# Performance work log

Hardware: AMD Instinct MI355X
Metric: run time of the kernel (lower is better)

## Reference

```python
import jax, jax.numpy as jnp
import numpy as np

NC, K, SD = 8, 1024, 64
L = NC * SD
B = 8192
TAU = 0.07
COMMIT_W = 1.0
CONTRAST_W = 1.0
EPS = 1e-12


def setup_inputs() -> dict:
    key = jax.random.key(0)
    kz, ke = jax.random.split(key)
    z = jax.random.normal(kz, (B, L), dtype=jnp.float32)
    embeddings = jax.random.normal(ke, (NC, K, SD), dtype=jnp.float32)
    return {"z": z, "embeddings": embeddings}


def reference(z, embeddings):
    sg = jax.lax.stop_gradient
    Bn, Ln = z.shape
    nc, k, sd = embeddings.shape
    zr = z.reshape(Bn, nc, sd)  # (B, nc, sd)

    # squared distances via ||z||^2 - 2 z.e + ||e||^2 -> (B, nc, K), avoids (B,nc,K,sd)
    z2 = jnp.sum(zr * zr, axis=-1)[:, :, None]
    e2 = jnp.sum(embeddings * embeddings, axis=-1)[None, :, :]
    cross = jnp.einsum('bnd,nkd->bnk', zr, embeddings)
    dists = z2 - 2.0 * cross + e2
    indices = jnp.argmin(dists, axis=-1)  # (B, nc)

    # codebook gather
    quant_splits = embeddings[jnp.arange(nc)[None, :], indices]  # (B, nc, sd)
    quant_z = quant_splits.reshape(Bn, Ln)

    commit_loss = jnp.mean((sg(quant_z) - z) ** 2)
    embed_loss = jnp.mean((quant_z - sg(z)) ** 2)
    total_commit = commit_loss + embed_loss

    quant_z_st = z + sg(quant_z - z)

    z_norm = z / jnp.maximum(jnp.linalg.norm(z, axis=-1, keepdims=True), EPS)
    q_det = sg(quant_z)
    q_norm = q_det / jnp.maximum(jnp.linalg.norm(q_det, axis=-1, keepdims=True), EPS)
    logits = jnp.matmul(q_norm, z_norm.T) / TAU  # (B, B)
    # cross-entropy with labels = arange(B)
    contrastive = jnp.mean(jax.nn.logsumexp(logits, axis=1) - jnp.diagonal(logits))

    return (quant_z_st, COMMIT_W * total_commit, CONTRAST_W * contrastive, indices)
```

## Files before the change

kernel.cpp:

```cpp
#include <hip/hip_runtime.h>
#include <cstdint>
#include <cstddef>

#define NCB   8
#define KC    1024
#define SDIM  64
#define LDIM  512
#define BATCH 8192
#define INV_TAU (1.0f/0.07f)
#define K2E  20.60992915555662f
#define DBIAS 256.0f

typedef __bf16 bf16_t;
typedef bf16_t bf16x8 __attribute__((ext_vector_type(8)));
typedef float  floatx4 __attribute__((ext_vector_type(4)));
typedef int    intx8  __attribute__((ext_vector_type(8)));
typedef unsigned int u32;

__device__ __forceinline__ unsigned short f2bf(float f) {
    union { float f; unsigned int u; } c; c.f = f;
    unsigned int u = c.u;
    u += 0x7fffu + ((u >> 16) & 1u);
    return (unsigned short)(u >> 16);
}
__device__ __forceinline__ float bf2f(unsigned short h) {
    union { unsigned int u; float f; } c; c.u = ((unsigned int)h) << 16;
    return c.f;
}
__device__ __forceinline__ float exp2_fast(float x) {
    float r; asm("v_exp_f32 %0, %1" : "=v"(r) : "v"(x)); return r;
}
__device__ __forceinline__ void gll16(const void* g, void* l) {
    __builtin_amdgcn_global_load_lds(
        (const __attribute__((address_space(1))) u32*)g,
        (__attribute__((address_space(3))) u32*)l,
        16, 0, 0);
}

__global__ __launch_bounds__(256) void
k_pre(const float* __restrict__ emb, float* __restrict__ e2,
      unsigned short* __restrict__ eh, unsigned short* __restrict__ el,
      float* __restrict__ accs) {
    int id = blockIdx.x * 256 + threadIdx.x;
    const float4* e4 = (const float4*)(emb + (size_t)id * SDIM);
    ushort4* eh4 = (ushort4*)(eh + (size_t)id * SDIM);
    ushort4* el4 = (ushort4*)(el + (size_t)id * SDIM);
    float s0=0.f,s1=0.f,s2=0.f,s3=0.f;
#pragma unroll
    for (int i=0;i<16;i++){ float4 v=e4[i];
        s0=fmaf(v.x,v.x,s0); s1=fmaf(v.y,v.y,s1);
        s2=fmaf(v.z,v.z,s2); s3=fmaf(v.w,v.w,s3);
        ushort4 h, l;
        h.x=f2bf(v.x); l.x=f2bf(v.x-bf2f(h.x));
        h.y=f2bf(v.y); l.y=f2bf(v.y-bf2f(h.y));
        h.z=f2bf(v.z); l.z=f2bf(v.z-bf2f(h.z));
        h.w=f2bf(v.w); l.w=f2bf(v.w-bf2f(h.w));
        eh4[i]=h; el4[i]=l;
    }
    e2[id] = (s0+s1)+(s2+s3);
    if (id==0){ accs[0]=0.f; accs[1]=0.f; accs[2]=0.f; }
}

__device__ __forceinline__ double dist64d(const float* __restrict__ e,
                                          const float* __restrict__ zg) {
    double se=0.0, sz=0.0;
#pragma unroll 8
    for (int i=0;i<64;i++){ double ev=(double)e[i];
        se = fma(ev,ev,se); sz = fma(ev,(double)zg[i],sz); }
    return se - 2.0*sz;
}

__global__ __launch_bounds__(256,2) void
k_argmin(const unsigned short* __restrict__ eh, const unsigned short* __restrict__ el,
         const float* __restrict__ e2, const float* __restrict__ z,
         const float* __restrict__ emb, float* __restrict__ out_q,
         float* __restrict__ out_idx, float* __restrict__ accs) {
    __shared__ __align__(16) unsigned short Ah[128*64], Al[128*64];
    __shared__ __align__(16) unsigned short Bh[2][64*64], Bl[2][64*64];
    __shared__ float e2s[2][64];
    __shared__ unsigned int mK[2][128][2];

    const int tid = threadIdx.x;
    const int n   = blockIdx.y;
    const int i0  = blockIdx.x * 128;
    const int wid = tid >> 6, lane = tid & 63;
    const int wm = wid & 1, wn = wid >> 1;
    const int c  = lane & 15, qq = lane >> 4;

#pragma unroll
    for (int s=0;s<8;s++){
        int seg = tid + s*256;
        int r = seg >> 4, sg = seg & 15;
        float4 v = *(const float4*)(z + (size_t)(i0+r)*LDIM + n*SDIM + sg*4);
        ushort4 h, l;
        h.x=f2bf(v.x); l.x=f2bf(v.x-bf2f(h.x));
        h.y=f2bf(v.y); l.y=f2bf(v.y-bf2f(h.y));
        h.z=f2bf(v.z); l.z=f2bf(v.z-bf2f(h.z));
        h.w=f2bf(v.w); l.w=f2bf(v.w-bf2f(h.w));
        int off = r*64 + ((sg*4) ^ ((r&7)<<3));
        *(ushort4*)(&Ah[off]) = h;
        *(ushort4*)(&Al[off]) = l;
    }

    const unsigned char* ehb = (const unsigned char*)(eh + (size_t)n*KC*SDIM);
    const unsigned char* elb = (const unsigned char*)(el + (size_t)n*KC*SDIM);
    const float* e2n = e2 + n*KC;

    const int brow = lane >> 3;
    const int bchk = ((lane & 7)*16) ^ (brow << 4);

    auto stageB = [&](int buf, int j0){
#pragma unroll
        for (int s=0;s<2;s++){
            int r0 = wid*16 + s*8;
            size_t go = (size_t)(j0 + r0 + brow)*128 + bchk;
            gll16(ehb + go, &Bh[buf][r0*64]);
            gll16(elb + go, &Bl[buf][r0*64]);
        }
    };

    if (tid < 64) e2s[0][tid] = e2n[tid] + DBIAS;
    stageB(0, 0);

    unsigned int k1[16], k2[16];
#pragma unroll
    for (int j=0;j<16;j++){ k1[j]=0xFFFFFFFFu; k2[j]=0xFFFFFFFFu; }

    __syncthreads();

    for (int jt=0; jt<16; jt++){
        const int cur = jt & 1, nxt = cur ^ 1;
        const int j0 = jt*64;
        float e2r = 0.f;
        if (jt < 15){
            stageB(nxt, j0 + 64);
            if (tid < 64) e2r = e2n[j0 + 64 + tid];
        }

        floatx4 acc[4][2];
#pragma unroll
        for (int mt=0;mt<4;mt++){
            acc[mt][0]=(floatx4){0.f,0.f,0.f,0.f};
            acc[mt][1]=(floatx4){0.f,0.f,0.f,0.f};
        }

#pragma unroll
        for (int t=0;t<2;t++){
            const int axo = (t*32 + qq*8) ^ ((c&7)<<3);
            bf16x8 ah[4], alo[4], bh[2], bl[2];
#pragma unroll
            for (int mt=0;mt<4;mt++){
                int ro = (wm*64 + mt*16 + c)*64 + axo;
                ah[mt]  = *(const bf16x8*)(&Ah[ro]);
                alo[mt] = *(const bf16x8*)(&Al[ro]);
            }
#pragma unroll
            for (int nt=0;nt<2;nt++){
                int ro = (wn*32 + nt*16 + c)*64 + axo;
                bh[nt] = *(const bf16x8*)(&Bh[cur][ro]);
                bl[nt] = *(const bf16x8*)(&Bl[cur][ro]);
            }
#pragma unroll
            for (int mt=0;mt<4;mt++)
#pragma unroll
                for (int nt=0;nt<2;nt++){
                    acc[mt][nt] = __builtin_amdgcn_mfma_f32_16x16x32_bf16(ah[mt],  bh[nt], acc[mt][nt], 0,0,0);
                    acc[mt][nt] = __builtin_amdgcn_mfma_f32_16x16x32_bf16(ah[mt],  bl[nt], acc[mt][nt], 0,0,0);
                    acc[mt][nt] = __builtin_amdgcn_mfma_f32_16x16x32_bf16(alo[mt], bh[nt], acc[mt][nt], 0,0,0);
                }
        }

#pragma unroll
        for (int nt=0;nt<2;nt++){
            const int colb = wn*32 + nt*16 + c;
            float e2v = e2s[cur][colb];
            unsigned int kidx = (unsigned int)(j0 + colb);
#pragma unroll
            for (int mt=0;mt<4;mt++)
#pragma unroll
                for (int reg=0;reg<4;reg++){
                    float d = fmaf(-2.0f, acc[mt][nt][reg], e2v);
                    unsigned int key = (__float_as_uint(d) & 0xFFFFFC00u) | kidx;
                    int s = mt*4+reg;
                    unsigned int o1 = k1[s], o2 = k2[s];
                    unsigned int nk2;
                    asm("v_med3_u32 %0, %1, %2, %3" : "=v"(nk2) : "v"(o1), "v"(o2), "v"(key));
                    k2[s] = nk2;
                    k1[s] = min(o1, key);
                }
        }

        if (jt < 15 && tid < 64) e2s[nxt][tid] = e2r + DBIAS;
        __syncthreads();
    }

#pragma unroll
    for (int off=1; off<16; off<<=1){
#pragma unroll
        for (int s=0;s<16;s++){
            unsigned int o1 = __shfl_xor(k1[s], off);
            unsigned int o2 = __shfl_xor(k2[s], off);
            unsigned int n1 = min(k1[s], o1);
            k2[s] = min( max(k1[s], o1), min(k2[s], o2) );
            k1[s] = n1;
        }
    }
    if (c == 0){
#pragma unroll
        for (int s=0;s<16;s++){
            int row = wm*64 + (s>>2)*16 + qq*4 + (s&3);
            mK[wn][row][0] = k1[s]; mK[wn][row][1] = k2[s];
        }
    }
    __syncthreads();

    if (tid < 128){
        int b = i0 + tid;
        unsigned int a1 = mK[0][tid][0], a2 = mK[0][tid][1];
        unsigned int c1 = mK[1][tid][0], c2 = mK[1][tid][1];
        unsigned int f1 = min(a1, c1);
        unsigned int f2 = min( max(a1, c1), min(a2, c2) );
        int ii1 = (int)(f1 & 0x3FFu);
        int ii2 = (int)(f2 & 0x3FFu);
        float d1q = __uint_as_float(f1 & 0xFFFFFC00u);
        float d2q = __uint_as_float(f2 & 0xFFFFFC00u);

        const float* eb = emb + (size_t)n*KC*SDIM;
        const float* zg = z + (size_t)b*LDIM + n*SDIM;
        if (d2q - d1q < 0.08f) {
            double d1 = dist64d(eb + (size_t)ii1*SDIM, zg);
            double d2 = dist64d(eb + (size_t)ii2*SDIM, zg);
            if (d2 < d1 || (d2 == d1 && ii2 < ii1)) ii1 = ii2;
        }

        const float4* q4 = (const float4*)(eb + (size_t)ii1*SDIM);
        const float4* z4 = (const float4*)zg;
        float4* oq = (float4*)(out_q + (size_t)b*LDIM + n*SDIM);
        float cs = 0.f;
#pragma unroll
        for (int i=0;i<16;i++){
            float4 v = q4[i]; float4 zv = z4[i];
            oq[i] = v;
            float d0=v.x-zv.x, d1=v.y-zv.y, d2=v.z-zv.z, d3=v.w-zv.w;
            cs += d0*d0 + d1*d1 + d2*d2 + d3*d3;
        }
        out_idx[b*NCB + n] = (float)ii1;

        for (int off=32; off; off>>=1) cs += __shfl_down(cs, off);
        if ((tid & 63)==0) atomicAdd(&accs[0], cs);
    }
}

__global__ __launch_bounds__(256) void
k_norm(const float* __restrict__ z, const float* __restrict__ q,
       unsigned char* __restrict__ zn8, unsigned char* __restrict__ qn8,
       float* __restrict__ diag) {
    const int b = blockIdx.x, tid = threadIdx.x;
    const size_t base = (size_t)b*LDIM;
    float2 zv = ((const float2*)(z+base))[tid];
    float2 qv = ((const float2*)(q+base))[tid];
    float sz = zv.x*zv.x + zv.y*zv.y;
    float sq = qv.x*qv.x + qv.y*qv.y;
    float sqz= qv.x*zv.x + qv.y*zv.y;
    for (int off=32; off; off>>=1){
        sz+=__shfl_down(sz,off); sq+=__shfl_down(sq,off); sqz+=__shfl_down(sqz,off);
    }
    __shared__ float red[3][4];
    __shared__ float bc[2];
    int w = tid>>6;
    if ((tid&63)==0){ red[0][w]=sz; red[1][w]=sq; red[2][w]=sqz; }
    __syncthreads();
    if (tid==0){
        float tz = red[0][0]+red[0][1]+red[0][2]+red[0][3];
        float tq = red[1][0]+red[1][1]+red[1][2]+red[1][3];
        float tz_q = red[2][0]+red[2][1]+red[2][2]+red[2][3];
        float inz = 1.0f/fmaxf(sqrtf(tz), 1e-12f);
        float inq = 1.0f/fmaxf(sqrtf(tq), 1e-12f);
        bc[0]=inz; bc[1]=inq;
        diag[b] = tz_q*inz*inq*INV_TAU;
    }
    __syncthreads();
    float inz=bc[0], inq=bc[1];
    int pz = __builtin_amdgcn_cvt_pk_fp8_f32(zv.x*inz, zv.y*inz, 0, false);
    int pq = __builtin_amdgcn_cvt_pk_fp8_f32(qv.x*inq, qv.y*inq, 0, false);
    ((unsigned short*)(zn8+base))[tid] = (unsigned short)(pz & 0xffff);
    ((unsigned short*)(qn8+base))[tid] = (unsigned short)(pq & 0xffff);
}

__global__ __launch_bounds__(256,2) void
k_logits(const unsigned char* __restrict__ qn8, const unsigned char* __restrict__ zn8,
         float* __restrict__ Spart) {
    __shared__ __align__(16) unsigned char Bs[2][64*512];
    const int tid  = threadIdx.x;
    const int i0   = blockIdx.x * 128;
    const int chnk = blockIdx.y;
    const int wid  = tid >> 6, lane = tid & 63;
    const int wm = wid & 1, wn = wid >> 1;
    const int c  = lane & 15, qq = lane >> 4;

    intx8 af[4][4];
#pragma unroll
    for (int mt=0;mt<4;mt++){
        const unsigned char* ap = qn8 + (size_t)(i0 + wm*64 + mt*16 + c)*LDIM + qq*32;
#pragma unroll
        for (int kc=0;kc<4;kc++){
            union { intx8 v; uint4 h[2]; } u;
            u.h[0] = *(const uint4*)(ap + kc*128);
            u.h[1] = *(const uint4*)(ap + kc*128 + 16);
            af[mt][kc] = u.v;
        }
    }

    const int brow  = lane >> 5;
    const int bchk0 = (lane & 31) * 16;

    auto stageB = [&](int buf, int j0){
#pragma unroll
        for (int s=0;s<8;s++){
            int r0  = wid*16 + s*2;
            int row = r0 + brow;
            gll16(zn8 + (size_t)(j0+row)*LDIM + (bchk0 ^ ((row&7)<<4)),
                  &Bs[buf][r0*512]);
        }
    };

    float S[16];
#pragma unroll
    for (int i=0;i<16;i++) S[i] = 0.f;

    stageB(0, chnk*1024);
    __syncthreads();

    for (int jt=0;jt<16;jt++){
        const int cur = jt & 1;
        const int j0 = chnk*1024 + jt*64;
        if (jt < 15) stageB(cur^1, j0 + 64);

        floatx4 acc[4][2];
#pragma unroll
        for (int mt=0;mt<4;mt++){
            acc[mt][0]=(floatx4){0.f,0.f,0.f,0.f};
            acc[mt][1]=(floatx4){0.f,0.f,0.f,0.f};
        }

#pragma unroll
        for (int kc=0;kc<4;kc++){
            intx8 bfr[2];
#pragma unroll
            for (int nt=0;nt<2;nt++){
                const unsigned char* p = &Bs[cur][(wn*32 + nt*16 + c)*512];
                const int o = kc*128 + qq*32;
                const int x = (c&7)<<4;
                union { intx8 v; uint4 h[2]; } u;
                u.h[0] = *(const uint4*)(p + (o ^ x));
                u.h[1] = *(const uint4*)(p + ((o + 16) ^ x));
                bfr[nt] = u.v;
            }
#pragma unroll
            for (int mt=0;mt<4;mt++)
#pragma unroll
                for (int nt=0;nt<2;nt++)
                    acc[mt][nt] = __builtin_amdgcn_mfma_scale_f32_16x16x128_f8f6f4(
                        af[mt][kc], bfr[nt], acc[mt][nt],
                        0, 0,
                        0, 127,
                        0, 127);
        }

#pragma unroll
        for (int mt=0;mt<4;mt++)
#pragma unroll
            for (int reg=0;reg<4;reg++){
                float e0 = exp2_fast(fmaf(acc[mt][0][reg], K2E, -K2E));
                float e1 = exp2_fast(fmaf(acc[mt][1][reg], K2E, -K2E));
                S[mt*4+reg] += e0 + e1;
            }
        __syncthreads();
    }

#pragma unroll
    for (int off=1; off<16; off<<=1)
#pragma unroll
        for (int s=0;s<16;s++) S[s] += __shfl_xor(S[s], off);

    if (c == 0){
        const int p = chnk*2 + wn;
#pragma unroll
        for (int mt=0;mt<4;mt++)
#pragma unroll
            for (int reg=0;reg<4;reg++){
                int row = i0 + wm*64 + mt*16 + qq*4 + reg;
                Spart[p*BATCH + row] = S[mt*4+reg];
            }
    }
}

__global__ __launch_bounds__(256) void
k_finalize(const float* __restrict__ Spart, const float* __restrict__ diag,
           float* __restrict__ accs, float* __restrict__ out_s) {
    int r = blockIdx.x*256 + threadIdx.x;
    float Ssum = 0.f;
#pragma unroll
    for (int p=0;p<16;p++) Ssum += Spart[p*BATCH + r];
    float val = INV_TAU + logf(Ssum) - diag[r];
    for (int off=32; off; off>>=1) val += __shfl_down(val, off);
    if ((threadIdx.x & 63)==0) atomicAdd(&accs[1], val);
    __syncthreads();
    if (threadIdx.x == 0){
        __threadfence();
        unsigned int old = __float_as_uint(atomicAdd(&accs[2], 1.0f));
        if (old == __float_as_uint(31.0f)) {
            __threadfence();
            float a0 = atomicAdd(&accs[0], 0.0f);
            float a1 = atomicAdd(&accs[1], 0.0f);
            out_s[0] = 2.0f*a0 / (float)((size_t)BATCH*LDIM);
            out_s[1] = a1 / (float)BATCH;
        }
    }
}

extern "C" void kernel_launch(void* const* d_in, const int* in_sizes, int n_in,
                              void* d_out, int out_size, void* d_ws, size_t ws_size,
                              hipStream_t stream) {
    const float* z   = (const float*)d_in[0];
    const float* emb = (const float*)d_in[1];
    float* out = (float*)d_out;
    float* out_q       = out;
    float* out_scalars = out + 4194304;
    float* out_idx     = out + 4194306;

    float* wsf   = (float*)d_ws;
    float* e2    = wsf;
    float* accs  = wsf + 8192;
    float* diag  = wsf + 8704;
    float* Spart = wsf + 16896;
    unsigned char* qn8 = (unsigned char*)(Spart + 32*BATCH);
    unsigned char* zn8 = qn8 + (size_t)BATCH*LDIM;
    unsigned short* eh = (unsigned short*)(zn8 + (size_t)BATCH*LDIM);
    unsigned short* el = eh + (size_t)NCB*KC*SDIM;

    k_pre    <<<32,          256, 0, stream>>>(emb, e2, eh, el, accs);
    k_argmin <<<dim3(64,8),  256, 0, stream>>>(eh, el, e2, z, emb,
                                               out_q, out_idx, accs);
    k_norm   <<<BATCH,       256, 0, stream>>>(z, out_q, zn8, qn8, diag);
    k_logits <<<dim3(64,8),  256, 0, stream>>>(qn8, zn8, Spart);
    k_finalize<<<32,         256, 0, stream>>>(Spart, diag, accs, out_scalars);
}
```

Before: 169.9 us.

## Load B operands directly from global into registers, drop LDS staging and barriers

In k_argmin and k_logits the double-buffered global_load_lds staging of the codebook/z tiles is removed; each warp now loads its MFMA B fragments directly from global memory (relying on L1/L2), and the per-iteration __syncthreads are gone. k_argmin's launch bounds are raised to allow three blocks per CU. This removes barrier stalls and LDS traffic and frees shared memory for occupancy. The cost is redundant global loads across warps and loss of explicit prefetch, which may expose memory latency.

```diff
diff --git a/kernel.cpp b/kernel.cpp
--- a/kernel.cpp
+++ b/kernel.cpp
@@ -29,12 +29,6 @@
 }
 __device__ __forceinline__ float exp2_fast(float x) {
     float r; asm("v_exp_f32 %0, %1" : "=v"(r) : "v"(x)); return r;
-}
-__device__ __forceinline__ void gll16(const void* g, void* l) {
-    __builtin_amdgcn_global_load_lds(
-        (const __attribute__((address_space(1))) u32*)g,
-        (__attribute__((address_space(3))) u32*)l,
-        16, 0, 0);
 }
 
 __global__ __launch_bounds__(256) void
@@ -70,14 +64,12 @@
     return se - 2.0*sz;
 }
 
-__global__ __launch_bounds__(256,2) void
+__global__ __launch_bounds__(256,3) void
 k_argmin(const unsigned short* __restrict__ eh, const unsigned short* __restrict__ el,
          const float* __restrict__ e2, const float* __restrict__ z,
          const float* __restrict__ emb, float* __restrict__ out_q,
          float* __restrict__ out_idx, float* __restrict__ accs) {
     __shared__ __align__(16) unsigned short Ah[128*64], Al[128*64];
-    __shared__ __align__(16) unsigned short Bh[2][64*64], Bl[2][64*64];
-    __shared__ float e2s[2][64];
     __shared__ unsigned int mK[2][128][2];
 
     const int tid = threadIdx.x;
@@ -102,26 +94,10 @@
         *(ushort4*)(&Al[off]) = l;
     }
 
-    const unsigned char* ehb = (const unsigned char*)(eh + (size_t)n*KC*SDIM);
-    const unsigned char* elb = (const unsigned char*)(el + (size_t)n*KC*SDIM);
+    const unsigned short* ehn = eh + (size_t)n*KC*SDIM;
+    const unsigned short* eln = el + (size_t)n*KC*SDIM;
     const float* e2n = e2 + n*KC;
 
-    const int brow = lane >> 3;
-    const int bchk = ((lane & 7)*16) ^ (brow << 4);
-
-    auto stageB = [&](int buf, int j0){
-#pragma unroll
-        for (int s=0;s<2;s++){
-            int r0 = wid*16 + s*8;
-            size_t go = (size_t)(j0 + r0 + brow)*128 + bchk;
-            gll16(ehb + go, &Bh[buf][r0*64]);
-            gll16(elb + go, &Bl[buf][r0*64]);
-        }
-    };
-
-    if (tid < 64) e2s[0][tid] = e2n[tid] + DBIAS;
-    stageB(0, 0);
-
     unsigned int k1[16], k2[16];
 #pragma unroll
     for (int j=0;j<16;j++){ k1[j]=0xFFFFFFFFu; k2[j]=0xFFFFFFFFu; }
@@ -129,12 +105,20 @@
     __syncthreads();
 
     for (int jt=0; jt<16; jt++){
-        const int cur = jt & 1, nxt = cur ^ 1;
         const int j0 = jt*64;
-        float e2r = 0.f;
-        if (jt < 15){
-            stageB(nxt, j0 + 64);
-            if (tid < 64) e2r = e2n[j0 + 64 + tid];
+
+        bf16x8 bh[2][2], bl[2][2];
+        float e2v[2];
+#pragma unroll
+        for (int nt=0;nt<2;nt++){
+            const int row = j0 + wn*32 + nt*16 + c;
+            const size_t rb = (size_t)row * SDIM;
+            e2v[nt] = e2n[row] + DBIAS;
+#pragma unroll
+            for (int t=0;t<2;t++){
+                bh[nt][t] = *(const bf16x8*)(ehn + rb + t*32 + qq*8);
+                bl[nt][t] = *(const bf16x8*)(eln + rb + t*32 + qq*8);
+            }
         }
 
         floatx4 acc[4][2];
@@ -147,7 +131,7 @@
 #pragma unroll
         for (int t=0;t<2;t++){
             const int axo = (t*32 + qq*8) ^ ((c&7)<<3);
-            bf16x8 ah[4], alo[4], bh[2], bl[2];
+            bf16x8 ah[4], alo[4];
 #pragma unroll
             for (int mt=0;mt<4;mt++){
                 int ro = (wm*64 + mt*16 + c)*64 + axo;
@@ -155,31 +139,24 @@
                 alo[mt] = *(const bf16x8*)(&Al[ro]);
             }
 #pragma unroll
-            for (int nt=0;nt<2;nt++){
-                int ro = (wn*32 + nt*16 + c)*64 + axo;
-                bh[nt] = *(const bf16x8*)(&Bh[cur][ro]);
-                bl[nt] = *(const bf16x8*)(&Bl[cur][ro]);
-            }
-#pragma unroll
             for (int mt=0;mt<4;mt++)
 #pragma unroll
                 for (int nt=0;nt<2;nt++){
-                    acc[mt][nt] = __builtin_amdgcn_mfma_f32_16x16x32_bf16(ah[mt],  bh[nt], acc[mt][nt], 0,0,0);
-                    acc[mt][nt] = __builtin_amdgcn_mfma_f32_16x16x32_bf16(ah[mt],  bl[nt], acc[mt][nt], 0,0,0);
-                    acc[mt][nt] = __builtin_amdgcn_mfma_f32_16x16x32_bf16(alo[mt], bh[nt], acc[mt][nt], 0,0,0);
+                    acc[mt][nt] = __builtin_amdgcn_mfma_f32_16x16x32_bf16(ah[mt],  bh[nt][t], acc[mt][nt], 0,0,0);
+                    acc[mt][nt] = __builtin_amdgcn_mfma_f32_16x16x32_bf16(ah[mt],  bl[nt][t], acc[mt][nt], 0,0,0);
+                    acc[mt][nt] = __builtin_amdgcn_mfma_f32_16x16x32_bf16(alo[mt], bh[nt][t], acc[mt][nt], 0,0,0);
                 }
         }
 
 #pragma unroll
         for (int nt=0;nt<2;nt++){
             const int colb = wn*32 + nt*16 + c;
-            float e2v = e2s[cur][colb];
             unsigned int kidx = (unsigned int)(j0 + colb);
 #pragma unroll
             for (int mt=0;mt<4;mt++)
 #pragma unroll
                 for (int reg=0;reg<4;reg++){
-                    float d = fmaf(-2.0f, acc[mt][nt][reg], e2v);
+                    float d = fmaf(-2.0f, acc[mt][nt][reg], e2v[nt]);
                     unsigned int key = (__float_as_uint(d) & 0xFFFFFC00u) | kidx;
                     int s = mt*4+reg;
                     unsigned int o1 = k1[s], o2 = k2[s];
@@ -189,9 +166,6 @@
                     k1[s] = min(o1, key);
                 }
         }
-
-        if (jt < 15 && tid < 64) e2s[nxt][tid] = e2r + DBIAS;
-        __syncthreads();
     }
 
 #pragma unroll
@@ -290,7 +264,6 @@
 __global__ __launch_bounds__(256,2) void
 k_logits(const unsigned char* __restrict__ qn8, const unsigned char* __restrict__ zn8,
          float* __restrict__ Spart) {
-    __shared__ __align__(16) unsigned char Bs[2][64*512];
     const int tid  = threadIdx.x;
     const int i0   = blockIdx.x * 128;
     const int chnk = blockIdx.y;
@@ -311,30 +284,24 @@
         }
     }
 
-    const int brow  = lane >> 5;
-    const int bchk0 = (lane & 31) * 16;
-
-    auto stageB = [&](int buf, int j0){
-#pragma unroll
-        for (int s=0;s<8;s++){
-            int r0  = wid*16 + s*2;
-            int row = r0 + brow;
-            gll16(zn8 + (size_t)(j0+row)*LDIM + (bchk0 ^ ((row&7)<<4)),
-                  &Bs[buf][r0*512]);
-        }
-    };
-
     float S[16];
 #pragma unroll
     for (int i=0;i<16;i++) S[i] = 0.f;
 
-    stageB(0, chnk*1024);
-    __syncthreads();
-
     for (int jt=0;jt<16;jt++){
-        const int cur = jt & 1;
         const int j0 = chnk*1024 + jt*64;
-        if (jt < 15) stageB(cur^1, j0 + 64);
+
+        const unsigned char* bp = zn8 + (size_t)(j0 + wn*32 + c)*LDIM + qq*32;
+        intx8 bfr[2][4];
+#pragma unroll
+        for (int nt=0;nt<2;nt++)
+#pragma unroll
+            for (int kc=0;kc<4;kc++){
+                union { intx8 v; uint4 h[2]; } u;
+                u.h[0] = *(const uint4*)(bp + (size_t)nt*16*LDIM + kc*128);
+                u.h[1] = *(const uint4*)(bp + (size_t)nt*16*LDIM + kc*128 + 16);
+                bfr[nt][kc] = u.v;
+            }
 
         floatx4 acc[4][2];
 #pragma unroll
@@ -344,28 +311,16 @@
         }
 
 #pragma unroll
-        for (int kc=0;kc<4;kc++){
-            intx8 bfr[2];
-#pragma unroll
-            for (int nt=0;nt<2;nt++){
-                const unsigned char* p = &Bs[cur][(wn*32 + nt*16 + c)*512];
-                const int o = kc*128 + qq*32;
-                const int x = (c&7)<<4;
-                union { intx8 v; uint4 h[2]; } u;
-                u.h[0] = *(const uint4*)(p + (o ^ x));
-                u.h[1] = *(const uint4*)(p + ((o + 16) ^ x));
-                bfr[nt] = u.v;
-            }
+        for (int kc=0;kc<4;kc++)
 #pragma unroll
             for (int mt=0;mt<4;mt++)
 #pragma unroll
                 for (int nt=0;nt<2;nt++)
                     acc[mt][nt] = __builtin_amdgcn_mfma_scale_f32_16x16x128_f8f6f4(
-                        af[mt][kc], bfr[nt], acc[mt][nt],
+                        af[mt][kc], bfr[nt][kc], acc[mt][nt],
                         0, 0,
                         0, 127,
                         0, 127);
-        }
 
 #pragma unroll
         for (int mt=0;mt<4;mt++)
@@ -375,7 +330,6 @@
                 float e1 = exp2_fast(fmaf(acc[mt][1][reg], K2E, -K2E));
                 S[mt*4+reg] += e0 + e1;
             }
-        __syncthreads();
     }
 
 #pragma unroll
```

After: 215.8 us. 27.0% more time.

## Keep argmin A tiles in registers and widen logits blocks to 512 threads

Applied to the files above, without the earlier changes.

In the argmin kernel, the z tile's bf16 hi/lo split now stays in registers instead of going through shared memory, and e2 is read straight from global memory. This removes the LDS staging buffers and per-tile LDS reads, and the occupancy hint is raised to 3 blocks. The logits kernel moves to 512 threads with 8 waves, each owning 32 rows, so each thread stages less B data and holds fewer accumulators. The trade-off is more register pressure in argmin and more threads sharing each block's barriers in logits.

```diff
diff --git a/kernel.cpp b/kernel.cpp
--- a/kernel.cpp
+++ b/kernel.cpp
@@ -70,14 +70,12 @@
     return se - 2.0*sz;
 }
 
-__global__ __launch_bounds__(256,2) void
+__global__ __launch_bounds__(256,3) void
 k_argmin(const unsigned short* __restrict__ eh, const unsigned short* __restrict__ el,
          const float* __restrict__ e2, const float* __restrict__ z,
          const float* __restrict__ emb, float* __restrict__ out_q,
          float* __restrict__ out_idx, float* __restrict__ accs) {
-    __shared__ __align__(16) unsigned short Ah[128*64], Al[128*64];
     __shared__ __align__(16) unsigned short Bh[2][64*64], Bl[2][64*64];
-    __shared__ float e2s[2][64];
     __shared__ unsigned int mK[2][128][2];
 
     const int tid = threadIdx.x;
@@ -87,21 +85,6 @@
     const int wm = wid & 1, wn = wid >> 1;
     const int c  = lane & 15, qq = lane >> 4;
 
-#pragma unroll
-    for (int s=0;s<8;s++){
-        int seg = tid + s*256;
-        int r = seg >> 4, sg = seg & 15;
-        float4 v = *(const float4*)(z + (size_t)(i0+r)*LDIM + n*SDIM + sg*4);
-        ushort4 h, l;
-        h.x=f2bf(v.x); l.x=f2bf(v.x-bf2f(h.x));
-        h.y=f2bf(v.y); l.y=f2bf(v.y-bf2f(h.y));
-        h.z=f2bf(v.z); l.z=f2bf(v.z-bf2f(h.z));
-        h.w=f2bf(v.w); l.w=f2bf(v.w-bf2f(h.w));
-        int off = r*64 + ((sg*4) ^ ((r&7)<<3));
-        *(ushort4*)(&Ah[off]) = h;
-        *(ushort4*)(&Al[off]) = l;
-    }
-
     const unsigned char* ehb = (const unsigned char*)(eh + (size_t)n*KC*SDIM);
     const unsigned char* elb = (const unsigned char*)(el + (size_t)n*KC*SDIM);
     const float* e2n = e2 + n*KC;
@@ -119,8 +102,30 @@
         }
     };
 
-    if (tid < 64) e2s[0][tid] = e2n[tid] + DBIAS;
     stageB(0, 0);
+
+    bf16x8 ah[4][2], al[4][2];
+#pragma unroll
+    for (int mt=0;mt<4;mt++)
+#pragma unroll
+        for (int t=0;t<2;t++){
+            const float* zr = z + (size_t)(i0 + wm*64 + mt*16 + c)*LDIM
+                                + n*SDIM + t*32 + qq*8;
+            float4 v0 = *(const float4*)(zr);
+            float4 v1 = *(const float4*)(zr + 4);
+            ushort4 h0, l0, h1, l1;
+            h0.x=f2bf(v0.x); l0.x=f2bf(v0.x-bf2f(h0.x));
+            h0.y=f2bf(v0.y); l0.y=f2bf(v0.y-bf2f(h0.y));
+            h0.z=f2bf(v0.z); l0.z=f2bf(v0.z-bf2f(h0.z));
+            h0.w=f2bf(v0.w); l0.w=f2bf(v0.w-bf2f(h0.w));
+            h1.x=f2bf(v1.x); l1.x=f2bf(v1.x-bf2f(h1.x));
+            h1.y=f2bf(v1.y); l1.y=f2bf(v1.y-bf2f(h1.y));
+            h1.z=f2bf(v1.z); l1.z=f2bf(v1.z-bf2f(h1.z));
+            h1.w=f2bf(v1.w); l1.w=f2bf(v1.w-bf2f(h1.w));
+            union { bf16x8 v; ushort4 u[2]; } uh, ul;
+            uh.u[0]=h0; uh.u[1]=h1; ul.u[0]=l0; ul.u[1]=l1;
+            ah[mt][t]=uh.v; al[mt][t]=ul.v;
+        }
 
     unsigned int k1[16], k2[16];
 #pragma unroll
@@ -131,11 +136,12 @@
     for (int jt=0; jt<16; jt++){
         const int cur = jt & 1, nxt = cur ^ 1;
         const int j0 = jt*64;
-        float e2r = 0.f;
-        if (jt < 15){
-            stageB(nxt, j0 + 64);
-            if (tid < 64) e2r = e2n[j0 + 64 + tid];
-        }
+        if (jt < 15) stageB(nxt, j0 + 64);
+
+        float e2v[2];
+#pragma unroll
+        for (int nt=0;nt<2;nt++)
+            e2v[nt] = e2n[j0 + wn*32 + nt*16 + c] + DBIAS;
 
         floatx4 acc[4][2];
 #pragma unroll
@@ -147,13 +153,7 @@
 #pragma unroll
         for (int t=0;t<2;t++){
             const int axo = (t*32 + qq*8) ^ ((c&7)<<3);
-            bf16x8 ah[4], alo[4], bh[2], bl[2];
-#pragma unroll
-            for (int mt=0;mt<4;mt++){
-                int ro = (wm*64 + mt*16 + c)*64 + axo;
-                ah[mt]  = *(const bf16x8*)(&Ah[ro]);
-                alo[mt] = *(const bf16x8*)(&Al[ro]);
-            }
+            bf16x8 bh[2], bl[2];
 #pragma unroll
             for (int nt=0;nt<2;nt++){
                 int ro = (wn*32 + nt*16 + c)*64 + axo;
@@ -164,22 +164,21 @@
             for (int mt=0;mt<4;mt++)
 #pragma unroll
                 for (int nt=0;nt<2;nt++){
-                    acc[mt][nt] = __builtin_amdgcn_mfma_f32_16x16x32_bf16(ah[mt],  bh[nt], acc[mt][nt], 0,0,0);
-                    acc[mt][nt] = __builtin_amdgcn_mfma_f32_16x16x32_bf16(ah[mt],  bl[nt], acc[mt][nt], 0,0,0);
-                    acc[mt][nt] = __builtin_amdgcn_mfma_f32_16x16x32_bf16(alo[mt], bh[nt], acc[mt][nt], 0,0,0);
+                    acc[mt][nt] = __builtin_amdgcn_mfma_f32_16x16x32_bf16(ah[mt][t], bh[nt], acc[mt][nt], 0,0,0);
+                    acc[mt][nt] = __builtin_amdgcn_mfma_f32_16x16x32_bf16(ah[mt][t], bl[nt], acc[mt][nt], 0,0,0);
+                    acc[mt][nt] = __builtin_amdgcn_mfma_f32_16x16x32_bf16(al[mt][t], bh[nt], acc[mt][nt], 0,0,0);
                 }
         }
 
 #pragma unroll
         for (int nt=0;nt<2;nt++){
             const int colb = wn*32 + nt*16 + c;
-            float e2v = e2s[cur][colb];
             unsigned int kidx = (unsigned int)(j0 + colb);
 #pragma unroll
             for (int mt=0;mt<4;mt++)
 #pragma unroll
                 for (int reg=0;reg<4;reg++){
-                    float d = fmaf(-2.0f, acc[mt][nt][reg], e2v);
+                    float d = fmaf(-2.0f, acc[mt][nt][reg], e2v[nt]);
                     unsigned int key = (__float_as_uint(d) & 0xFFFFFC00u) | kidx;
                     int s = mt*4+reg;
                     unsigned int o1 = k1[s], o2 = k2[s];
@@ -189,8 +188,6 @@
                     k1[s] = min(o1, key);
                 }
         }
-
-        if (jt < 15 && tid < 64) e2s[nxt][tid] = e2r + DBIAS;
         __syncthreads();
     }
 
@@ -287,7 +284,7 @@
     ((unsigned short*)(qn8+base))[tid] = (unsigned short)(pq & 0xffff);
 }
 
-__global__ __launch_bounds__(256,2) void
+__global__ __launch_bounds__(512,4) void
 k_logits(const unsigned char* __restrict__ qn8, const unsigned char* __restrict__ zn8,
          float* __restrict__ Spart) {
     __shared__ __align__(16) unsigned char Bs[2][64*512];
@@ -295,13 +292,28 @@
     const int i0   = blockIdx.x * 128;
     const int chnk = blockIdx.y;
     const int wid  = tid >> 6, lane = tid & 63;
-    const int wm = wid & 1, wn = wid >> 1;
+    const int wm = wid & 3, wn = wid >> 2;
     const int c  = lane & 15, qq = lane >> 4;
 
-    intx8 af[4][4];
-#pragma unroll
-    for (int mt=0;mt<4;mt++){
-        const unsigned char* ap = qn8 + (size_t)(i0 + wm*64 + mt*16 + c)*LDIM + qq*32;
+    const int brow  = lane >> 5;
+    const int bchk0 = (lane & 31) * 16;
+
+    auto stageB = [&](int buf, int j0){
+#pragma unroll
+        for (int s=0;s<4;s++){
+            int r0  = wid*8 + s*2;
+            int row = r0 + brow;
+            gll16(zn8 + (size_t)(j0+row)*LDIM + (bchk0 ^ ((row&7)<<4)),
+                  &Bs[buf][r0*512]);
+        }
+    };
+
+    stageB(0, chnk*1024);
+
+    intx8 af[2][4];
+#pragma unroll
+    for (int mt=0;mt<2;mt++){
+        const unsigned char* ap = qn8 + (size_t)(i0 + wm*32 + mt*16 + c)*LDIM + qq*32;
 #pragma unroll
         for (int kc=0;kc<4;kc++){
             union { intx8 v; uint4 h[2]; } u;
@@ -311,24 +323,10 @@
         }
     }
 
-    const int brow  = lane >> 5;
-    const int bchk0 = (lane & 31) * 16;
-
-    auto stageB = [&](int buf, int j0){
-#pragma unroll
-        for (int s=0;s<8;s++){
-            int r0  = wid*16 + s*2;
-            int row = r0 + brow;
-            gll16(zn8 + (size_t)(j0+row)*LDIM + (bchk0 ^ ((row&7)<<4)),
-                  &Bs[buf][r0*512]);
-        }
-    };
-
-    float S[16];
-#pragma unroll
-    for (int i=0;i<16;i++) S[i] = 0.f;
-
-    stageB(0, chnk*1024);
+    float S[8];
+#pragma unroll
+    for (int i=0;i<8;i++) S[i] = 0.f;
+
     __syncthreads();
 
     for (int jt=0;jt<16;jt++){
@@ -336,9 +334,9 @@
         const int j0 = chnk*1024 + jt*64;
         if (jt < 15) stageB(cur^1, j0 + 64);
 
-        floatx4 acc[4][2];
-#pragma unroll
-        for (int mt=0;mt<4;mt++){
+        floatx4 acc[2][2];
+#pragma unroll
+        for (int mt=0;mt<2;mt++){
             acc[mt][0]=(floatx4){0.f,0.f,0.f,0.f};
             acc[mt][1]=(floatx4){0.f,0.f,0.f,0.f};
         }
@@ -348,16 +346,17 @@
             intx8 bfr[2];
 #pragma unroll
             for (int nt=0;nt<2;nt++){
-                const unsigned char* p = &Bs[cur][(wn*32 + nt*16 + c)*512];
+                const int rb = wn*32 + nt*16 + c;
+                const unsigned char* p = &Bs[cur][rb*512];
                 const int o = kc*128 + qq*32;
-                const int x = (c&7)<<4;
+                const int x = (rb&7)<<4;
                 union { intx8 v; uint4 h[2]; } u;
                 u.h[0] = *(const uint4*)(p + (o ^ x));
                 u.h[1] = *(const uint4*)(p + ((o + 16) ^ x));
                 bfr[nt] = u.v;
             }
 #pragma unroll
-            for (int mt=0;mt<4;mt++)
+            for (int mt=0;mt<2;mt++)
 #pragma unroll
                 for (int nt=0;nt<2;nt++)
                     acc[mt][nt] = __builtin_amdgcn_mfma_scale_f32_16x16x128_f8f6f4(
@@ -368,7 +367,7 @@
         }
 
 #pragma unroll
-        for (int mt=0;mt<4;mt++)
+        for (int mt=0;mt<2;mt++)
 #pragma unroll
             for (int reg=0;reg<4;reg++){
                 float e0 = exp2_fast(fmaf(acc[mt][0][reg], K2E, -K2E));
@@ -381,15 +380,15 @@
 #pragma unroll
     for (int off=1; off<16; off<<=1)
 #pragma unroll
-        for (int s=0;s<16;s++) S[s] += __shfl_xor(S[s], off);
+        for (int s=0;s<8;s++) S[s] += __shfl_xor(S[s], off);
 
     if (c == 0){
         const int p = chnk*2 + wn;
 #pragma unroll
-        for (int mt=0;mt<4;mt++)
+        for (int mt=0;mt<2;mt++)
 #pragma unroll
             for (int reg=0;reg<4;reg++){
-                int row = i0 + wm*64 + mt*16 + qq*4 + reg;
+                int row = i0 + wm*32 + mt*16 + qq*4 + reg;
                 Spart[p*BATCH + row] = S[mt*4+reg];
             }
     }
@@ -443,6 +442,6 @@
     k_argmin <<<dim3(64,8),  256, 0, stream>>>(eh, el, e2, z, emb,
                                                out_q, out_idx, accs);
     k_norm   <<<BATCH,       256, 0, stream>>>(z, out_q, zn8, qn8, diag);
-    k_logits <<<dim3(64,8),  256, 0, stream>>>(qn8, zn8, Spart);
+    k_logits <<<dim3(64,8),  512, 0, stream>>>(qn8, zn8, Spart);
     k_finalize<<<32,         256, 0, stream>>>(Spart, diag, accs, out_scalars);
 }
```

Result: slower. 184.3 us (+8.5%).
